# Kernel optimization log

Hardware: AMD Instinct MI355X
Metric: run time of the kernel (lower is better)

## Reference

```python
import jax, jax.numpy as jnp
import numpy as np

N_HEADS = 4
NS_STEPS = 5
NS_EPS = 1e-7

def newtonschulz5(G):
    # G: [out, in]; quintic Newton-Schulz, 5 steps. out==in here so no transpose branch needed,
    # but keep the static-shape check for faithfulness.
    a, b, c = 3.4445, -4.775, 2.0315
    X = G / (jnp.linalg.norm(G) + NS_EPS)
    transposed = G.shape[0] > G.shape[1]
    if transposed:
        X = X.T
    def step(X, _):
        A = X @ X.T
        B = b * A + c * (A @ A)
        return a * X + B @ X, None
    X, _ = jax.lax.scan(step, X, None, length=NS_STEPS)
    if transposed:
        X = X.T
    return X

def setup_inputs() -> dict:
    key = jax.random.key(0)
    k1, k2, k3, k4, k5 = jax.random.split(key, 5)
    B, S, D_in, D_out, r = 4, 2048, 4096, 4096, 16
    init_std = 0.01 / np.sqrt(D_out * r)
    return {
        "x": jax.random.normal(k1, (B, S, D_in), dtype=jnp.float32),
        "W": jax.random.normal(k2, (D_out, D_in), dtype=jnp.float32) * 0.02,
        "bias": jax.random.normal(k3, (D_out,), dtype=jnp.float32) * 0.02,
        "lora_A": jax.random.normal(k4, (r, D_in), dtype=jnp.float32),
        "lora_B": jax.random.normal(k5, (D_out, r), dtype=jnp.float32) * init_std,
    }

def reference(x, W, bias, lora_A, lora_B):
    # base linear (frozen weights); dropout is identity (p=0 / eval)
    base_out = jnp.einsum('bsi,oi->bso', x, W) + bias
    r, D_in = lora_A.shape
    D_out = lora_B.shape[0]
    hr = r // N_HEADS
    Ah = lora_A.reshape(N_HEADS, hr, D_in)                       # [h, hr, in]
    Bh = lora_B.reshape(D_out, N_HEADS, hr).transpose(1, 0, 2)    # [h, out, hr]
    G = jnp.einsum('hor,hri->hoi', Bh, Ah)                        # [h, out, in]
    alpha = jnp.sqrt(jnp.sum(G * G, axis=(1, 2)))                 # per-head Frobenius norm
    M = jax.vmap(newtonschulz5)(G)                                # [h, out, in]
    lora_out = jnp.einsum('h,hoi,bsi->bso', alpha, M, x)
    return base_out + lora_out
```

## Files before the change

kernel.cpp:

```cpp
#include <hip/hip_runtime.h>
#include <math.h>

#define MDIM 8192
#define NDIM 4096
#define KDIM 4096

typedef __attribute__((ext_vector_type(8))) _Float16 h8;
typedef __attribute__((ext_vector_type(4))) _Float16 h4;
typedef __attribute__((ext_vector_type(4))) float f32x4;

typedef const __attribute__((address_space(1))) void* gas_ptr;
typedef __attribute__((address_space(3))) void* las_ptr;

__device__ inline void load16_to_lds(const void* g, void* l) {
  __builtin_amdgcn_global_load_lds((gas_ptr)g, (las_ptr)l, 16, 0, 0);
}

__device__ inline void mm4(const double* A, const double* B, double* C) {
#pragma unroll
  for (int p = 0; p < 4; ++p)
#pragma unroll
    for (int q = 0; q < 4; ++q) {
      double s = 0.0;
#pragma unroll
      for (int r = 0; r < 4; ++r) s += A[p * 4 + r] * B[r * 4 + q];
      C[p * 4 + q] = s;
    }
}
__device__ inline void mm4_bt(const double* A, const double* B, double* C) {
#pragma unroll
  for (int p = 0; p < 4; ++p)
#pragma unroll
    for (int q = 0; q < 4; ++q) {
      double s = 0.0;
#pragma unroll
      for (int r = 0; r < 4; ++r) s += A[p * 4 + r] * B[q * 4 + r];
      C[p * 4 + q] = s;
    }
}

__global__ void ns_kernel(const float* __restrict__ lora_A,
                          const float* __restrict__ lora_B,
                          float* __restrict__ E) {
  const int h = blockIdx.x;
  const int tid = threadIdx.x;
  const int lane = tid & 63;
  const int wave = tid >> 6;

  float gu[16], gv[16];
#pragma unroll
  for (int e = 0; e < 16; ++e) { gu[e] = 0.f; gv[e] = 0.f; }

  for (int o = tid; o < NDIM; o += 256) {
    const float4 bv = *(const float4*)(lora_B + (size_t)o * 16 + h * 4);
    const float bb[4] = {bv.x, bv.y, bv.z, bv.w};
#pragma unroll
    for (int p = 0; p < 4; ++p)
#pragma unroll
      for (int q = 0; q < 4; ++q) gu[p * 4 + q] += bb[p] * bb[q];
  }
  for (int i = tid; i < KDIM; i += 256) {
    float aa[4];
#pragma unroll
    for (int p = 0; p < 4; ++p) aa[p] = lora_A[(size_t)(h * 4 + p) * KDIM + i];
#pragma unroll
    for (int p = 0; p < 4; ++p)
#pragma unroll
      for (int q = 0; q < 4; ++q) gv[p * 4 + q] += aa[p] * aa[q];
  }

#pragma unroll
  for (int e = 0; e < 16; ++e) {
#pragma unroll
    for (int off = 32; off > 0; off >>= 1) {
      gu[e] += __shfl_down(gu[e], off, 64);
      gv[e] += __shfl_down(gv[e], off, 64);
    }
  }
  __shared__ float pu[4][16], pv[4][16];
  if (lane == 0) {
#pragma unroll
    for (int e = 0; e < 16; ++e) { pu[wave][e] = gu[e]; pv[wave][e] = gv[e]; }
  }
  __syncthreads();

  if (tid == 0) {
    double gud[16], gvd[16];
#pragma unroll
    for (int e = 0; e < 16; ++e) {
      gud[e] = (double)pu[0][e] + pu[1][e] + pu[2][e] + pu[3][e];
      gvd[e] = (double)pv[0][e] + pv[1][e] + pv[2][e] + pv[3][e];
    }
    double tr = 0.0;
#pragma unroll
    for (int e = 0; e < 16; ++e) tr += gud[e] * gvd[e];
    const double alpha = sqrt(tr);
    const double n0 = alpha + 1e-7;

    double C[16] = {0};
    C[0] = C[5] = C[10] = C[15] = 1.0 / n0;

    const double a = 3.4445, b = -4.775, c = 2.0315;
    for (int it = 0; it < 5; ++it) {
      double T1[16], D[16], DG[16], DGD[16], GuC[16], F[16], Cn[16];
      mm4(C, gvd, T1);
      mm4_bt(T1, C, D);
      mm4(D, gud, DG);
      mm4(DG, D, DGD);
      mm4(gud, C, GuC);
#pragma unroll
      for (int e = 0; e < 16; ++e) F[e] = b * D[e] + c * DGD[e];
      mm4(F, GuC, Cn);
#pragma unroll
      for (int e = 0; e < 16; ++e) C[e] = a * C[e] + Cn[e];
    }
#pragma unroll
    for (int e = 0; e < 16; ++e) E[h * 16 + e] = (float)(alpha * C[e]);
  }
}

__global__ void prep_kernel(const float* __restrict__ x,
                            const float* __restrict__ W,
                            const float* __restrict__ lora_A,
                            const float* __restrict__ lora_B,
                            const float* __restrict__ E,
                            _Float16* __restrict__ Wh,
                            _Float16* __restrict__ Xh) {
  const int tid = threadIdx.x;
  if (blockIdx.x < 256) {
    __shared__ float cf[16][16];
    __shared__ __align__(16) float Asm[16][1024];
    const int o0 = blockIdx.x * 16;
    {
      const int r = tid >> 4, kk = tid & 15, h = kk >> 2, q = kk & 3;
      float s = 0.f;
#pragma unroll
      for (int p = 0; p < 4; ++p)
        s += lora_B[(size_t)(o0 + r) * 16 + h * 4 + p] * E[h * 16 + p * 4 + q];
      cf[r][kk] = s;
    }
    for (int kb = 0; kb < KDIM; kb += 1024) {
      __syncthreads();
#pragma unroll
      for (int j = 0; j < 16; ++j) {
        const int f4 = tid + j * 256;
        const int k = f4 >> 8, c4 = f4 & 255;
        *(float4*)&Asm[k][c4 * 4] =
            *(const float4*)&lora_A[(size_t)k * KDIM + kb + (size_t)c4 * 4];
      }
      __syncthreads();
      float4 av[16];
#pragma unroll
      for (int k = 0; k < 16; ++k) av[k] = *(const float4*)&Asm[k][tid * 4];
#pragma unroll
      for (int r = 0; r < 16; ++r) {
        const size_t base = (size_t)(o0 + r) * KDIM + kb + tid * 4;
        float4 acc = *(const float4*)&W[base];
#pragma unroll
        for (int k = 0; k < 16; ++k) {
          const float cfv = cf[r][k];
          acc.x += cfv * av[k].x; acc.y += cfv * av[k].y;
          acc.z += cfv * av[k].z; acc.w += cfv * av[k].w;
        }
        h4 pk;
        pk[0] = (_Float16)acc.x; pk[1] = (_Float16)acc.y;
        pk[2] = (_Float16)acc.z; pk[3] = (_Float16)acc.w;
        *(h4*)(Wh + base) = pk;
      }
    }
  } else {
    const size_t t = (size_t)(blockIdx.x - 256) * 256 + tid;
    const size_t base = t * 8;
    const float4 a = *(const float4*)(x + base);
    const float4 b = *(const float4*)(x + base + 4);
    h8 o;
    o[0] = (_Float16)a.x; o[1] = (_Float16)a.y; o[2] = (_Float16)a.z; o[3] = (_Float16)a.w;
    o[4] = (_Float16)b.x; o[5] = (_Float16)b.y; o[6] = (_Float16)b.z; o[7] = (_Float16)b.w;
    *(h8*)(Xh + base) = o;
  }
}

__launch_bounds__(512, 2)
__global__ void gemm_kernel(const _Float16* __restrict__ Xh,
                            const _Float16* __restrict__ Wh,
                            const float* __restrict__ bias,
                            float* __restrict__ out) {
  __shared__ __align__(16) _Float16 sA0_0[128 * 64], sA0_1[128 * 64];
  __shared__ __align__(16) _Float16 sA1_0[128 * 64], sA1_1[128 * 64];
  __shared__ __align__(16) _Float16 sB0_0[128 * 64], sB0_1[128 * 64];
  __shared__ __align__(16) _Float16 sB1_0[128 * 64], sB1_1[128 * 64];

  const int tid = threadIdx.x;
  const int lane = tid & 63;
  const int wave = tid >> 6;
  const int wm = wave >> 2;
  const int wn = wave & 3;
  const int quad = lane >> 4;
  const int r16 = lane & 15;
  const int sw = r16 & 7;

  const int lin = blockIdx.x;
  const int wg = (lin & 7) * 64 + (lin >> 3);
  const int bm = wg >> 4;
  const int bn = wg & 15;

  const int row0 = tid >> 3;
  const int lc0 = (tid & 7) ^ (row0 & 7);
  const size_t off0 = (size_t)row0 * KDIM + lc0 * 8;
  const int ldsb = tid * 16;
  const _Float16* pA0 = Xh + (size_t)(bm * 256) * KDIM;
  const _Float16* pA1 = pA0 + (size_t)128 * KDIM;
  const _Float16* pB0 = Wh + (size_t)(bn * 256) * KDIM;
  const _Float16* pB1 = pB0 + (size_t)128 * KDIM;

  const int aRow = (wm * 64 + r16) * 64;
  const int bRow = (wn * 32 + r16) * 64;
  const int c0 = (quad ^ sw) * 8;
  const int c1 = ((quad + 4) ^ sw) * 8;

  f32x4 acc[2][2][4][2] = {};
  h8 a0[4][2], a1[4][2], b0[2][2], b1[2][2];

#define STAGE(arr, p, koff) do {                                               \
    load16_to_lds((p) + off0 + (koff), (char*)(arr) + ldsb);                   \
    load16_to_lds((p) + off0 + (size_t)64 * KDIM + (koff),                     \
                  (char*)(arr) + ldsb + 8192);                                 \
  } while (0)

#define FENCE() asm volatile("" ::: "memory")
#define BAR() do { FENCE(); __builtin_amdgcn_s_barrier(); FENCE(); } while (0)
#define VM4() asm volatile("s_waitcnt vmcnt(4)" ::: "memory")
#define VM2() asm volatile("s_waitcnt vmcnt(2)" ::: "memory")
#define VM0() asm volatile("s_waitcnt vmcnt(0)" ::: "memory")

#define RDA(dst, Aarr) do { _Pragma("unroll")                                  \
    for (int f = 0; f < 4; ++f) {                                              \
      dst[f][0] = *(const h8*)&Aarr[aRow + f * 1024 + c0];                     \
      dst[f][1] = *(const h8*)&Aarr[aRow + f * 1024 + c1];                     \
    } } while (0)
#define RDB(dst, Barr) do { _Pragma("unroll")                                  \
    for (int g = 0; g < 2; ++g) {                                              \
      dst[g][0] = *(const h8*)&Barr[bRow + g * 1024 + c0];                     \
      dst[g][1] = *(const h8*)&Barr[bRow + g * 1024 + c1];                     \
    } } while (0)

#define MFMA16(MQ, NQ, AV, BV) do {                                            \
    __builtin_amdgcn_s_setprio(1);                                             \
    _Pragma("unroll")                                                          \
    for (int f = 0; f < 4; ++f)                                                \
      _Pragma("unroll")                                                        \
      for (int g = 0; g < 2; ++g) {                                            \
        acc[MQ][NQ][f][g] = __builtin_amdgcn_mfma_f32_16x16x32_f16(            \
            AV[f][0], BV[g][0], acc[MQ][NQ][f][g], 0, 0, 0);                   \
        acc[MQ][NQ][f][g] = __builtin_amdgcn_mfma_f32_16x16x32_f16(            \
            AV[f][1], BV[g][1], acc[MQ][NQ][f][g], 0, 0, 0);                   \
      }                                                                        \
    __builtin_amdgcn_s_setprio(0);                                             \
  } while (0)

#define TILE(t, cA0, cA1, cB0, cB1, nA0, nA1, nB0, nB1) do {                   \
    RDA(a0, cA0); RDB(b0, cB0); STAGE(nA0, pA0, ((t) + 1) * 64);               \
    BAR(); MFMA16(0, 0, a0, b0); VM4(); BAR();                                 \
    RDB(b1, cB1);                STAGE(nB0, pB0, ((t) + 1) * 64);              \
    BAR(); MFMA16(0, 1, a0, b1); VM4(); BAR();                                 \
    RDA(a1, cA1);                STAGE(nB1, pB1, ((t) + 1) * 64);              \
    BAR(); MFMA16(1, 1, a1, b1);        BAR();                                 \
    RDB(b0, cB0);                STAGE(nA1, pA1, ((t) + 1) * 64);              \
    BAR(); MFMA16(1, 0, a1, b0); VM4(); BAR();                                 \
  } while (0)

#define TILE_LAST(cA0, cA1, cB0, cB1) do {                                     \
    RDA(a0, cA0); RDB(b0, cB0);                                                \
    BAR(); MFMA16(0, 0, a0, b0); VM2(); BAR();                                 \
    RDB(b1, cB1);                                                              \
    BAR(); MFMA16(0, 1, a0, b1); VM0(); BAR();                                 \
    RDA(a1, cA1);                                                              \
    BAR(); MFMA16(1, 1, a1, b1);        BAR();                                 \
    RDB(b0, cB0);                                                              \
    BAR(); MFMA16(1, 0, a1, b0);        BAR();                                 \
  } while (0)

  constexpr int NT = KDIM / 64;

  STAGE(sA0_0, pA0, 0);
  STAGE(sB0_0, pB0, 0);
  STAGE(sB1_0, pB1, 0);
  STAGE(sA1_0, pA1, 0);
  VM4();
  BAR();

#pragma unroll 1
  for (int t2 = 0; t2 < NT - 2; t2 += 2) {
    TILE(t2,     sA0_0, sA1_0, sB0_0, sB1_0, sA0_1, sA1_1, sB0_1, sB1_1);
    TILE(t2 + 1, sA0_1, sA1_1, sB0_1, sB1_1, sA0_0, sA1_0, sB0_0, sB1_0);
  }
  TILE(NT - 2, sA0_0, sA1_0, sB0_0, sB1_0, sA0_1, sA1_1, sB0_1, sB1_1);
  TILE_LAST(sA0_1, sA1_1, sB0_1, sB1_1);

#pragma unroll
  for (int mq = 0; mq < 2; ++mq)
#pragma unroll
    for (int f = 0; f < 4; ++f) {
      float* po = out + (size_t)(bm * 256 + mq * 128 + wm * 64 + f * 16 + quad * 4) * NDIM;
#pragma unroll
      for (int nq = 0; nq < 2; ++nq)
#pragma unroll
        for (int g = 0; g < 2; ++g) {
          const int ocol = bn * 256 + nq * 128 + wn * 32 + g * 16 + r16;
          const float bb = bias[ocol];
          const f32x4 v = acc[mq][nq][f][g];
#pragma unroll
          for (int rg = 0; rg < 4; ++rg)
            po[(size_t)rg * NDIM + ocol] = v[rg] + bb;
        }
    }
}

extern "C" void kernel_launch(void* const* d_in, const int* in_sizes, int n_in,
                              void* d_out, int out_size, void* d_ws, size_t ws_size,
                              hipStream_t stream) {
  const float* x      = (const float*)d_in[0];
  const float* W      = (const float*)d_in[1];
  const float* bias   = (const float*)d_in[2];
  const float* lora_A = (const float*)d_in[3];
  const float* lora_B = (const float*)d_in[4];
  float* out = (float*)d_out;

  char* ws = (char*)d_ws;
  float* E = (float*)ws;
  _Float16* Wh = (_Float16*)(ws + 1024);
  _Float16* Xh = (_Float16*)(ws + 1024 + (size_t)NDIM * KDIM * 2);

  ns_kernel<<<dim3(4), dim3(256), 0, stream>>>(lora_A, lora_B, E);
  prep_kernel<<<dim3(256 + (MDIM * KDIM) / (256 * 8)), dim3(256), 0, stream>>>(
      x, W, lora_A, lora_B, E, Wh, Xh);
  gemm_kernel<<<dim3(512), dim3(512), 0, stream>>>(Xh, Wh, bias, out);
}
```

Measured before the change: 602.9 us.

## Deepen GEMM prefetch pipeline and split weight-prep blocks along K

```diff
diff --git a/kernel.cpp b/kernel.cpp
--- a/kernel.cpp
+++ b/kernel.cpp
@@ -127,10 +127,11 @@
                             _Float16* __restrict__ Wh,
                             _Float16* __restrict__ Xh) {
   const int tid = threadIdx.x;
-  if (blockIdx.x < 256) {
+  if (blockIdx.x < 512) {
     __shared__ float cf[16][16];
     __shared__ __align__(16) float Asm[16][1024];
-    const int o0 = blockIdx.x * 16;
+    const int o0 = (blockIdx.x >> 1) * 16;
+    const int kh = (blockIdx.x & 1) * 2048;
     {
       const int r = tid >> 4, kk = tid & 15, h = kk >> 2, q = kk & 3;
       float s = 0.f;
@@ -139,7 +140,7 @@
         s += lora_B[(size_t)(o0 + r) * 16 + h * 4 + p] * E[h * 16 + p * 4 + q];
       cf[r][kk] = s;
     }
-    for (int kb = 0; kb < KDIM; kb += 1024) {
+    for (int kb = kh; kb < kh + 2048; kb += 1024) {
       __syncthreads();
 #pragma unroll
       for (int j = 0; j < 16; ++j) {
@@ -169,7 +170,7 @@
       }
     }
   } else {
-    const size_t t = (size_t)(blockIdx.x - 256) * 256 + tid;
+    const size_t t = (size_t)(blockIdx.x - 512) * 256 + tid;
     const size_t base = t * 8;
     const float4 a = *(const float4*)(x + base);
     const float4 b = *(const float4*)(x + base + 4);
@@ -229,9 +230,7 @@
 
 #define FENCE() asm volatile("" ::: "memory")
 #define BAR() do { FENCE(); __builtin_amdgcn_s_barrier(); FENCE(); } while (0)
-#define VM4() asm volatile("s_waitcnt vmcnt(4)" ::: "memory")
-#define VM2() asm volatile("s_waitcnt vmcnt(2)" ::: "memory")
-#define VM0() asm volatile("s_waitcnt vmcnt(0)" ::: "memory")
+#define VMC(n) asm volatile("s_waitcnt vmcnt(" #n ")" ::: "memory")
 
 #define RDA(dst, Aarr) do { _Pragma("unroll")                                  \
     for (int f = 0; f < 4; ++f) {                                              \
@@ -258,44 +257,66 @@
     __builtin_amdgcn_s_setprio(0);                                             \
   } while (0)
 
-#define TILE(t, cA0, cA1, cB0, cB1, nA0, nA1, nB0, nB1) do {                   \
-    RDA(a0, cA0); RDB(b0, cB0); STAGE(nA0, pA0, ((t) + 1) * 64);               \
-    BAR(); MFMA16(0, 0, a0, b0); VM4(); BAR();                                 \
-    RDB(b1, cB1);                STAGE(nB0, pB0, ((t) + 1) * 64);              \
-    BAR(); MFMA16(0, 1, a0, b1); VM4(); BAR();                                 \
-    RDA(a1, cA1);                STAGE(nB1, pB1, ((t) + 1) * 64);              \
-    BAR(); MFMA16(1, 1, a1, b1);        BAR();                                 \
-    RDB(b0, cB0);                STAGE(nA1, pA1, ((t) + 1) * 64);              \
-    BAR(); MFMA16(1, 0, a1, b0); VM4(); BAR();                                 \
-  } while (0)
-
-#define TILE_LAST(cA0, cA1, cB0, cB1) do {                                     \
-    RDA(a0, cA0); RDB(b0, cB0);                                                \
-    BAR(); MFMA16(0, 0, a0, b0); VM2(); BAR();                                 \
-    RDB(b1, cB1);                                                              \
-    BAR(); MFMA16(0, 1, a0, b1); VM0(); BAR();                                 \
-    RDA(a1, cA1);                                                              \
-    BAR(); MFMA16(1, 1, a1, b1);        BAR();                                 \
-    RDB(b0, cB0);                                                              \
-    BAR(); MFMA16(1, 0, a1, b0);        BAR();                                 \
-  } while (0)
-
-  constexpr int NT = KDIM / 64;
+#define PH(PRE, STG, MQ, NQ, AV, BV, VMW) do {                                 \
+    BAR();                                                                     \
+    PRE;                                                                       \
+    STG;                                                                       \
+    __builtin_amdgcn_sched_barrier(0);                                         \
+    MFMA16(MQ, NQ, AV, BV);                                                    \
+    VMW;                                                                       \
+  } while (0)
+
+#define NOP() do { } while (0)
+
+#define TILE_EVEN(t) do {                                                      \
+    PH(RDB(b1, sB1_0), STAGE(sA1_1, pA1, ((t) + 1) * 64), 0, 0, a0, b0, VMC(8)); \
+    PH(RDA(a1, sA1_0), STAGE(sA0_0, pA0, ((t) + 2) * 64), 0, 1, a0, b1, NOP()); \
+    PH(NOP(),          STAGE(sB0_0, pB0, ((t) + 2) * 64), 1, 1, a1, b1, VMC(6)); \
+    PH({ RDA(a0, sA0_1); RDB(b1, sB1_1); },                                    \
+                       STAGE(sB1_0, pB1, ((t) + 2) * 64), 1, 0, a1, b0, NOP()); \
+  } while (0)
+
+#define TILE_ODD(t) do {                                                       \
+    PH(RDB(b0, sB0_1), STAGE(sA1_0, pA1, ((t) + 1) * 64), 0, 1, a0, b1, VMC(8)); \
+    PH(RDA(a1, sA1_1), STAGE(sA0_1, pA0, ((t) + 2) * 64), 0, 0, a0, b0, NOP()); \
+    PH(NOP(),          STAGE(sB0_1, pB0, ((t) + 2) * 64), 1, 0, a1, b0, VMC(6)); \
+    PH({ RDA(a0, sA0_0); RDB(b0, sB0_0); },                                    \
+                       STAGE(sB1_1, pB1, ((t) + 2) * 64), 1, 1, a1, b1, NOP()); \
+  } while (0)
+
+#define TILE_62() do {                                                         \
+    PH(RDB(b1, sB1_0), STAGE(sA1_1, pA1, 63 * 64), 0, 0, a0, b0, VMC(8));      \
+    PH(RDA(a1, sA1_0), NOP(),                      0, 1, a0, b1, NOP());       \
+    PH(NOP(),          NOP(),                      1, 1, a1, b1, VMC(2));      \
+    PH({ RDA(a0, sA0_1); RDB(b1, sB1_1); }, NOP(), 1, 0, a1, b0, NOP());       \
+  } while (0)
+
+#define TILE_63() do {                                                         \
+    PH(RDB(b0, sB0_1), NOP(), 0, 1, a0, b1, VMC(0));                           \
+    PH(RDA(a1, sA1_1), NOP(), 0, 0, a0, b0, NOP());                            \
+    PH(NOP(),          NOP(), 1, 0, a1, b0, NOP());                           \
+    PH(NOP(),          NOP(), 1, 1, a1, b1, NOP());                           \
+  } while (0)
 
   STAGE(sA0_0, pA0, 0);
   STAGE(sB0_0, pB0, 0);
   STAGE(sB1_0, pB1, 0);
   STAGE(sA1_0, pA1, 0);
-  VM4();
+  STAGE(sA0_1, pA0, 64);
+  STAGE(sB0_1, pB0, 64);
+  STAGE(sB1_1, pB1, 64);
+  VMC(8);
   BAR();
+  RDA(a0, sA0_0);
+  RDB(b0, sB0_0);
 
 #pragma unroll 1
-  for (int t2 = 0; t2 < NT - 2; t2 += 2) {
-    TILE(t2,     sA0_0, sA1_0, sB0_0, sB1_0, sA0_1, sA1_1, sB0_1, sB1_1);
-    TILE(t2 + 1, sA0_1, sA1_1, sB0_1, sB1_1, sA0_0, sA1_0, sB0_0, sB1_0);
-  }
-  TILE(NT - 2, sA0_0, sA1_0, sB0_0, sB1_0, sA0_1, sA1_1, sB0_1, sB1_1);
-  TILE_LAST(sA0_1, sA1_1, sB0_1, sB1_1);
+  for (int t2 = 0; t2 < 62; t2 += 2) {
+    TILE_EVEN(t2);
+    TILE_ODD(t2 + 1);
+  }
+  TILE_62();
+  TILE_63();
 
 #pragma unroll
   for (int mq = 0; mq < 2; ++mq)
@@ -332,7 +353,7 @@
   _Float16* Xh = (_Float16*)(ws + 1024 + (size_t)NDIM * KDIM * 2);
 
   ns_kernel<<<dim3(4), dim3(256), 0, stream>>>(lora_A, lora_B, E);
-  prep_kernel<<<dim3(256 + (MDIM * KDIM) / (256 * 8)), dim3(256), 0, stream>>>(
+  prep_kernel<<<dim3(512 + (MDIM * KDIM) / (256 * 8)), dim3(256), 0, stream>>>(
       x, W, lora_A, lora_B, E, Wh, Xh);
   gemm_kernel<<<dim3(512), dim3(512), 0, stream>>>(Xh, Wh, bias, out);
 }
```

Result: slower. 912.9 us (+51.4%).
